# Kernel optimization log

Hardware: AMD Instinct MI355X
Metric: run time of the kernel (lower is better)

Reference implementation:

```python
import jax, jax.numpy as jnp
import numpy as np

N_NODES = 10000
N_EDGES = 50000
H = 64  # hidden channels


def _glorot(key, shape):
    fan_in = shape[0]
    return jax.random.normal(key, shape, dtype=jnp.float32) / jnp.sqrt(jnp.float32(fan_in))


def setup_inputs() -> dict:
    key = jax.random.key(0)
    ks = jax.random.split(key, 16)
    x = jax.random.normal(ks[0], (N_NODES, 20), dtype=jnp.float32)
    edge_index = jax.random.randint(ks[1], (2, N_EDGES), 0, N_NODES, dtype=jnp.int64)
    edge_attr = jax.random.uniform(ks[2], (N_EDGES, 5), dtype=jnp.float32)
    vpa = jax.random.normal(ks[3], (1,), dtype=jnp.float32)
    mz = jax.random.normal(ks[4], (1,), dtype=jnp.float32)
    adduct = jax.random.normal(ks[5], (3,), dtype=jnp.float32)
    params = {
        'lin0_w': _glorot(ks[6], (20, H)), 'lin0_b': jnp.zeros((H,), jnp.float32),
        'nn1_w': _glorot(ks[7], (5, H)), 'nn1_b': jnp.zeros((H,), jnp.float32),
        'nn2_w': _glorot(ks[8], (H, H * H)), 'nn2_b': jnp.zeros((H * H,), jnp.float32),
        'root_w': _glorot(ks[9], (H, H)), 'conv_b': jnp.zeros((H,), jnp.float32),
        'bneck_w': _glorot(ks[10], (H + 2 + 3, 384)), 'bneck_b': jnp.zeros((384,), jnp.float32),
        'lin1_w': _glorot(ks[11], (384, 384)), 'lin1_b': jnp.zeros((384,), jnp.float32),
        'lin2_w': _glorot(ks[12], (384, 1)), 'lin2_b': jnp.zeros((1,), jnp.float32),
    }
    return dict(x=x, edge_index=edge_index, edge_attr=edge_attr, vpa=vpa, mz=mz,
                adduct=adduct, **params)


def reference(x, edge_index, edge_attr, vpa, mz, adduct,
              lin0_w, lin0_b, nn1_w, nn1_b, nn2_w, nn2_b, root_w, conv_b,
              bneck_w, bneck_b, lin1_w, lin1_b, lin2_w, lin2_b):
    n = x.shape[0]
    src, dst = edge_index[0], edge_index[1]

    h = jax.nn.relu(x @ lin0_w + lin0_b)  # [N,64]

    # Edge-conditioned weights (edge_attr is loop-invariant -> compute once).
    e_hidden = jax.nn.relu(edge_attr @ nn1_w + nn1_b)          # [E,64]
    w_edge = (e_hidden @ nn2_w + nn2_b).reshape(-1, H, H)      # [E,64,64]

    # mean-aggregation denominator (in-degree, clamped to >=1)
    deg = jax.ops.segment_sum(jnp.ones_like(dst, dtype=h.dtype), dst,
                              num_segments=n)
    denom = jnp.maximum(deg, 1.0)[:, None]                     # [N,1]

    for _ in range(3):  # graph_conv_N
        msg = jnp.einsum('ei,eio->eo', h[src], w_edge)         # [E,64]
        agg = jax.ops.segment_sum(msg, dst, num_segments=n) / denom
        h = jax.nn.relu(h @ root_w + agg + conv_b)

    out_g = jnp.sum(h, axis=0)                                  # [64]
    out = jnp.concatenate([out_g, vpa, mz, adduct], axis=-1)    # [69]
    out = jax.nn.relu(out @ bneck_w + bneck_b)                  # [384]
    for _ in range(6):  # MLP_N
        out = jax.nn.relu(out @ lin1_w + lin1_b)
    return out @ lin2_w + lin2_b                                # [1]
```

## Files before the change

### kernel.cpp

```cpp
#include <hip/hip_runtime.h>
#include <stdint.h>

#define NN 10000
#define NE 50000
#define KTOT 4224
#define SPLITK 11
#define KCH 384
#define NSTEP 12
#define KPAD 200

typedef __attribute__((ext_vector_type(8))) _Float16 f16x8;
typedef __attribute__((ext_vector_type(4))) float f32x4;

__global__ void k_lin0(const float* __restrict__ x, const float* __restrict__ w,
                       const float* __restrict__ b, float* __restrict__ h) {
  int idx = blockIdx.x * blockDim.x + threadIdx.x;
  if (idx >= NN * 64) return;
  int n = idx >> 6, o = idx & 63;
  float acc = b[o];
  const float* xr = x + n * 20;
#pragma unroll
  for (int j = 0; j < 20; ++j) acc += xr[j] * w[j * 64 + o];
  h[idx] = acc > 0.f ? acc : 0.f;
}

__global__ void k_eh(const float* __restrict__ ea, const float* __restrict__ w,
                     const float* __restrict__ b, float* __restrict__ u) {
  int idx = blockIdx.x * blockDim.x + threadIdx.x;
  if (idx >= NE * 64) return;
  int e = idx >> 6, o = idx & 63;
  float acc = b[o];
  const float* er = ea + e * 5;
#pragma unroll
  for (int j = 0; j < 5; ++j) acc += er[j] * w[j * 64 + o];
  u[idx] = acc > 0.f ? acc : 0.f;
}

__global__ void k_deg(const int* __restrict__ ei, int* __restrict__ deg) {
  int e = blockIdx.x * blockDim.x + threadIdx.x;
  if (e < NE) atomicAdd(&deg[ei[NE + e]], 1);
}

__global__ void k_scan(const int* __restrict__ deg, int* __restrict__ offs,
                       float* __restrict__ inv_denom) {
  __shared__ int s[256];
  int t = threadIdx.x;
  int base = t * 40;
  int sum = 0;
  for (int j = 0; j < 40; ++j) {
    int n = base + j;
    sum += (n < NN) ? deg[n] : 0;
  }
  s[t] = sum;
  __syncthreads();
  for (int off = 1; off < 256; off <<= 1) {
    int v = (t >= off) ? s[t - off] : 0;
    __syncthreads();
    s[t] += v;
    __syncthreads();
  }
  int run = s[t] - sum;
  for (int j = 0; j < 40; ++j) {
    int n = base + j;
    if (n < NN) {
      offs[n] = run;
      int d = deg[n];
      run += d;
      inv_denom[n] = 1.0f / (float)(d > 0 ? d : 1);
    }
  }
  if (t == 255) offs[NN] = s[255];
}

__global__ void k_csr(const int* __restrict__ ei, const int* __restrict__ offs,
                      int* __restrict__ cursor, int* __restrict__ csr_src,
                      int* __restrict__ csr_eid) {
  int e = blockIdx.x * blockDim.x + threadIdx.x;
  if (e >= NE) return;
  int d = ei[NE + e];
  int pos = offs[d] + atomicAdd(&cursor[d], 1);
  csr_src[pos] = ei[e];
  csr_eid[pos] = e;
}

__global__ void k_wf(const float* __restrict__ w2, const float* __restrict__ b2,
                     const float* __restrict__ rootw, _Float16* __restrict__ wh,
                     _Float16* __restrict__ wl) {
  int idx = blockIdx.x * blockDim.x + threadIdx.x;
  if (idx >= 64 * KTOT) return;
  int o = idx / KTOT, c = idx - o * KTOT;
  float v;
  if (c < 4096) {
    v = w2[(c >> 6) * 4096 + (c & 63) * 64 + o];
  } else if (c < 4160) {
    v = b2[(c - 4096) * 64 + o];
  } else {
    v = rootw[(c - 4160) * 64 + o];
  }
  _Float16 hi = (_Float16)v;
  wh[idx] = hi;
  wl[idx] = (_Float16)(v - (float)hi);
}

__global__ void __launch_bounds__(256) k_scatter(
    const float* __restrict__ h, const float* __restrict__ u,
    const int* __restrict__ offs, const int* __restrict__ csr_src,
    const int* __restrict__ csr_eid, const float* __restrict__ inv_denom,
    _Float16* __restrict__ sv16, int chunk_start, int chunk_nodes) {
  __shared__ float hrow_s[4][2][64];
  int t = threadIdx.x;
  int wid = t >> 6, lane = t & 63;
  int n_local = blockIdx.x * 4 + wid;
  if (n_local >= chunk_nodes) return;
  int n = chunk_start + n_local;
  int beg = offs[n], end = offs[n + 1];
  int nE = end - beg;
  float invd = inv_denom[n];
  float acc[64];
#pragma unroll
  for (int i = 0; i < 64; ++i) acc[i] = 0.f;
  float hsacc = 0.f;
  float uk_c = 0.f, hv_c = 0.f;
  int eid_n = 0, src_n = 0;
  if (nE > 0) {
    int e0 = csr_eid[beg], s0 = csr_src[beg];
    uk_c = u[(size_t)e0 * 64 + lane];
    hv_c = h[(size_t)s0 * 64 + lane];
    hrow_s[wid][0][lane] = hv_c;
    if (nE > 1) { eid_n = csr_eid[beg + 1]; src_n = csr_src[beg + 1]; }
  }
  for (int c = 0; c < nE; ++c) {
    float uk_nn = 0.f, hv_nn = 0.f;
    if (c + 1 < nE) {
      uk_nn = u[(size_t)eid_n * 64 + lane];
      hv_nn = h[(size_t)src_n * 64 + lane];
    }
    if (c + 2 < nE) { eid_n = csr_eid[beg + c + 2]; src_n = csr_src[beg + c + 2]; }
    hsacc += hv_c;
    float uk = uk_c;
    const float* rowp = &hrow_s[wid][c & 1][0];
#pragma unroll
    for (int j = 0; j < 16; ++j) {
      float4 h4 = *(const float4*)&rowp[j * 4];
      acc[j * 4 + 0] += uk * h4.x;
      acc[j * 4 + 1] += uk * h4.y;
      acc[j * 4 + 2] += uk * h4.z;
      acc[j * 4 + 3] += uk * h4.w;
    }
    if (c + 1 < nE) hrow_s[wid][(c + 1) & 1][lane] = hv_nn;
    uk_c = uk_nn; hv_c = hv_nn;
  }
  size_t rowo = (size_t)n_local * KTOT + (size_t)lane * 64;
#pragma unroll
  for (int j = 0; j < 8; ++j) {
    f16x8 v;
#pragma unroll
    for (int q = 0; q < 8; ++q) v[q] = (_Float16)(acc[j * 8 + q] * invd);
    *(f16x8*)(sv16 + rowo + j * 8) = v;
  }
  size_t base = (size_t)n_local * KTOT;
  sv16[base + 4096 + lane] = (_Float16)(hsacc * invd);
  sv16[base + 4160 + lane] = (_Float16)(h[(size_t)n * 64 + lane]);
}

__global__ void __launch_bounds__(256) k_mfma(
    const _Float16* __restrict__ sv16, const _Float16* __restrict__ wh,
    const _Float16* __restrict__ wl, float* __restrict__ part,
    int chunk_start, int chunk_nodes) {
  __shared__ _Float16 Bh_s[64 * KPAD];
  __shared__ _Float16 Bl_s[64 * KPAD];
  int t = threadIdx.x;
  int wid = t >> 6, lane = t & 63;
  int node0 = blockIdx.x * 128;
  int kc = blockIdx.y;
  int r16 = lane & 15, kg = lane >> 4;
  int row0 = node0 + wid * 16 + r16;
  int row1 = row0 + 64;
  int rg0 = row0 < chunk_nodes ? row0 : (chunk_nodes - 1);
  int rg1 = row1 < chunk_nodes ? row1 : (chunk_nodes - 1);
  const _Float16* pa0 = sv16 + (size_t)rg0 * KTOT + kg * 8;
  const _Float16* pa1 = sv16 + (size_t)rg1 * KTOT + kg * 8;
  f32x4 p0 = {0.f, 0.f, 0.f, 0.f}, p1 = p0, p2 = p0, p3 = p0;
  f32x4 q0 = p0, q1 = p0, q2 = p0, q3 = p0;
  const int kb0 = kc * KCH;
  f16x8 a0 = *(const f16x8*)(pa0 + kb0);
  f16x8 a1 = *(const f16x8*)(pa1 + kb0);
  const int lb = r16 * KPAD + kg * 8;
#pragma unroll 1
  for (int ks = 0; ks < NSTEP; ++ks) {
    if ((ks == 0) || (ks == 6)) {
      __syncthreads();
      int gb = kb0 + (ks >> 1) * 32 * 0 + (ks / 6) * 192;
#pragma unroll
      for (int j = 0; j < 6; ++j) {
        int c = j * 256 + t;
        int o = c / 24, kk = (c - o * 24) * 8;
        *(f16x8*)&Bh_s[o * KPAD + kk] = *(const f16x8*)&wh[(size_t)o * KTOT + gb + kk];
        *(f16x8*)&Bl_s[o * KPAD + kk] = *(const f16x8*)&wl[(size_t)o * KTOT + gb + kk];
      }
      __syncthreads();
    }
    int kb = kb0 + ks * 32;
    int kbn = kb + ((ks + 1 < NSTEP) ? 32 : 0);
    int lk = lb + (ks % 6) * 32;
    f16x8 bh0 = *(const f16x8*)&Bh_s[lk];
    f16x8 bh1 = *(const f16x8*)&Bh_s[lk + 16 * KPAD];
    f16x8 bh2 = *(const f16x8*)&Bh_s[lk + 32 * KPAD];
    f16x8 bh3 = *(const f16x8*)&Bh_s[lk + 48 * KPAD];
    f16x8 bl0 = *(const f16x8*)&Bl_s[lk];
    f16x8 bl1 = *(const f16x8*)&Bl_s[lk + 16 * KPAD];
    f16x8 bl2 = *(const f16x8*)&Bl_s[lk + 32 * KPAD];
    f16x8 bl3 = *(const f16x8*)&Bl_s[lk + 48 * KPAD];
    f16x8 n0 = *(const f16x8*)(pa0 + kbn);
    f16x8 n1 = *(const f16x8*)(pa1 + kbn);
    p0 = __builtin_amdgcn_mfma_f32_16x16x32_f16(a0, bh0, p0, 0, 0, 0);
    p1 = __builtin_amdgcn_mfma_f32_16x16x32_f16(a0, bh1, p1, 0, 0, 0);
    p2 = __builtin_amdgcn_mfma_f32_16x16x32_f16(a0, bh2, p2, 0, 0, 0);
    p3 = __builtin_amdgcn_mfma_f32_16x16x32_f16(a0, bh3, p3, 0, 0, 0);
    p0 = __builtin_amdgcn_mfma_f32_16x16x32_f16(a0, bl0, p0, 0, 0, 0);
    p1 = __builtin_amdgcn_mfma_f32_16x16x32_f16(a0, bl1, p1, 0, 0, 0);
    p2 = __builtin_amdgcn_mfma_f32_16x16x32_f16(a0, bl2, p2, 0, 0, 0);
    p3 = __builtin_amdgcn_mfma_f32_16x16x32_f16(a0, bl3, p3, 0, 0, 0);
    q0 = __builtin_amdgcn_mfma_f32_16x16x32_f16(a1, bh0, q0, 0, 0, 0);
    q1 = __builtin_amdgcn_mfma_f32_16x16x32_f16(a1, bh1, q1, 0, 0, 0);
    q2 = __builtin_amdgcn_mfma_f32_16x16x32_f16(a1, bh2, q2, 0, 0, 0);
    q3 = __builtin_amdgcn_mfma_f32_16x16x32_f16(a1, bh3, q3, 0, 0, 0);
    q0 = __builtin_amdgcn_mfma_f32_16x16x32_f16(a1, bl0, q0, 0, 0, 0);
    q1 = __builtin_amdgcn_mfma_f32_16x16x32_f16(a1, bl1, q1, 0, 0, 0);
    q2 = __builtin_amdgcn_mfma_f32_16x16x32_f16(a1, bl2, q2, 0, 0, 0);
    q3 = __builtin_amdgcn_mfma_f32_16x16x32_f16(a1, bl3, q3, 0, 0, 0);
    a0 = n0; a1 = n1;
  }
  float* pp0 = part + (size_t)kc * NN * 64 +
               (size_t)(chunk_start + node0 + wid * 16) * 64;
  float* pp1 = pp0 + (size_t)64 * 64;
  int rbase = kg * 4;
#pragma unroll
  for (int j = 0; j < 4; ++j) {
    int row = rbase + j;
    if (node0 + wid * 16 + row < chunk_nodes) {
      pp0[row * 64 + 0  + r16] = p0[j];
      pp0[row * 64 + 16 + r16] = p1[j];
      pp0[row * 64 + 32 + r16] = p2[j];
      pp0[row * 64 + 48 + r16] = p3[j];
    }
    if (node0 + 64 + wid * 16 + row < chunk_nodes) {
      pp1[row * 64 + 0  + r16] = q0[j];
      pp1[row * 64 + 16 + r16] = q1[j];
      pp1[row * 64 + 32 + r16] = q2[j];
      pp1[row * 64 + 48 + r16] = q3[j];
    }
  }
}

__global__ void k_epi(const float* __restrict__ part, const float* __restrict__ cb,
                      float* __restrict__ hout) {
  int idx4 = blockIdx.x * blockDim.x + threadIdx.x;
  if (idx4 >= NN * 16) return;
  int o4 = (idx4 & 15) * 4;
  float4 a = make_float4(cb[o4], cb[o4 + 1], cb[o4 + 2], cb[o4 + 3]);
#pragma unroll
  for (int kc = 0; kc < SPLITK; ++kc) {
    float4 pv = *(const float4*)&part[(size_t)kc * NN * 64 + (size_t)idx4 * 4];
    a.x += pv.x; a.y += pv.y; a.z += pv.z; a.w += pv.w;
  }
  float4 r = make_float4(a.x > 0.f ? a.x : 0.f, a.y > 0.f ? a.y : 0.f,
                         a.z > 0.f ? a.z : 0.f, a.w > 0.f ? a.w : 0.f);
  *(float4*)&hout[(size_t)idx4 * 4] = r;
}

__global__ void k_sum_p(const float* __restrict__ h, float* __restrict__ part) {
  __shared__ float s[256];
  int t = threadIdx.x, b = blockIdx.x;
  int o = t & 63, g = t >> 6;
  float acc = 0.f;
  for (int k = 0;; ++k) {
    int n = b + 160 * (g + 4 * k);
    if (n >= NN) break;
    acc += h[(size_t)n * 64 + o];
  }
  s[t] = acc;
  __syncthreads();
  if (t < 64) part[(size_t)b * 64 + t] = s[t] + s[64 + t] + s[128 + t] + s[192 + t];
}

__global__ void __launch_bounds__(384) k_bneck(
    const float* __restrict__ part, const float* __restrict__ vpa,
    const float* __restrict__ mz, const float* __restrict__ adduct,
    const float* __restrict__ bw, const float* __restrict__ bb,
    float* __restrict__ aout) {
  __shared__ float in69[69];
  __shared__ float red[256];
  int t = threadIdx.x;
  if (t < 256) {
    int o = t & 63, g = t >> 6;
    float acc = 0.f;
    for (int k = 0; k < 40; ++k) acc += part[(size_t)(g * 40 + k) * 64 + o];
    red[t] = acc;
  }
  __syncthreads();
  if (t < 64) in69[t] = red[t] + red[64 + t] + red[128 + t] + red[192 + t];
  if (t == 64) in69[64] = vpa[0];
  if (t == 65) in69[65] = mz[0];
  if (t >= 66 && t < 69) in69[t] = adduct[t - 66];
  __syncthreads();
  float acc = bb[t];
#pragma unroll 4
  for (int i = 0; i < 69; ++i) acc += in69[i] * bw[i * 384 + t];
  aout[t] = acc > 0.f ? acc : 0.f;
}

__global__ void __launch_bounds__(256) k_layer(
    const float* __restrict__ ain, const float* __restrict__ w,
    const float* __restrict__ bias, float* __restrict__ aout) {
  __shared__ float a_s[384];
  __shared__ float red[256];
  int t = threadIdx.x;
  for (int i = t; i < 384; i += 256) a_s[i] = ain[i];
  __syncthreads();
  int o = blockIdx.x * 16 + (t & 15);
  int ig = t >> 4;
  float acc = 0.f;
#pragma unroll
  for (int k = 0; k < 24; ++k) {
    int i = ig + (k << 4);
    acc += a_s[i] * w[i * 384 + o];
  }
  red[t] = acc;
  __syncthreads();
  if (t < 128) red[t] += red[t + 128];
  __syncthreads();
  if (t < 64) red[t] += red[t + 64];
  __syncthreads();
  if (t < 32) red[t] += red[t + 32];
  __syncthreads();
  if (t < 16) {
    float v = red[t] + red[t + 16] + bias[o];
    aout[o] = v > 0.f ? v : 0.f;
  }
}

__global__ void __launch_bounds__(384) k_out(
    const float* __restrict__ act, const float* __restrict__ l2w,
    const float* __restrict__ l2b, float* __restrict__ out) {
  __shared__ float red[384];
  int t = threadIdx.x;
  red[t] = act[t] * l2w[t];
  __syncthreads();
  if (t < 128) red[t] += red[t + 128] + red[t + 256];
  __syncthreads();
  if (t < 64) {
    float s2 = red[t] + red[t + 64];
#pragma unroll
    for (int off = 32; off; off >>= 1) s2 += __shfl_down(s2, off);
    if (t == 0) out[0] = s2 + l2b[0];
  }
}

extern "C" void kernel_launch(void* const* d_in, const int* in_sizes, int n_in,
                              void* d_out, int out_size, void* d_ws, size_t ws_size,
                              hipStream_t stream) {
  const float* x      = (const float*)d_in[0];
  const int* ei       = (const int*)d_in[1];
  const float* ea     = (const float*)d_in[2];
  const float* vpa    = (const float*)d_in[3];
  const float* mz     = (const float*)d_in[4];
  const float* adduct = (const float*)d_in[5];
  const float* lin0_w = (const float*)d_in[6];
  const float* lin0_b = (const float*)d_in[7];
  const float* nn1_w  = (const float*)d_in[8];
  const float* nn1_b  = (const float*)d_in[9];
  const float* nn2_w  = (const float*)d_in[10];
  const float* nn2_b  = (const float*)d_in[11];
  const float* root_w = (const float*)d_in[12];
  const float* conv_b = (const float*)d_in[13];
  const float* bw     = (const float*)d_in[14];
  const float* bb     = (const float*)d_in[15];
  const float* l1w    = (const float*)d_in[16];
  const float* l1b    = (const float*)d_in[17];
  const float* l2w    = (const float*)d_in[18];
  const float* l2b    = (const float*)d_in[19];

  char* p = (char*)d_ws;
  auto alloc = [&](size_t bytes) {
    char* r = p;
    p += (bytes + 255) & ~(size_t)255;
    return r;
  };
  float* h0      = (float*)alloc((size_t)NN * 64 * 4);
  float* h1      = (float*)alloc((size_t)NN * 64 * 4);
  float* u       = (float*)alloc((size_t)NE * 64 * 4);
  _Float16* wh   = (_Float16*)alloc((size_t)64 * KTOT * 2);
  _Float16* wl   = (_Float16*)alloc((size_t)64 * KTOT * 2);
  int* deg       = (int*)alloc(NN * 4);
  int* offs      = (int*)alloc((NN + 1) * 4);
  int* cursor    = (int*)alloc(NN * 4);
  float* invd    = (float*)alloc(NN * 4);
  int* csr_src   = (int*)alloc(NE * 4);
  int* csr_eid   = (int*)alloc(NE * 4);
  float* part    = (float*)alloc(160 * 64 * 4);
  float* kpart   = (float*)alloc((size_t)SPLITK * NN * 64 * 4);
  float* actA    = (float*)alloc(384 * 4);
  float* actB    = (float*)alloc(384 * 4);
  size_t used = (size_t)(p - (char*)d_ws);
  size_t avail = ws_size > used ? ws_size - used : 0;
  long long CH = (long long)(avail / ((size_t)KTOT * 2));
  if (CH > NN) CH = NN;
  if (CH < 1) CH = 1;
  _Float16* sv16 = (_Float16*)p;

  hipMemsetAsync(deg, 0, NN * 4, stream);
  hipMemsetAsync(cursor, 0, NN * 4, stream);

  k_lin0<<<(NN * 64 + 255) / 256, 256, 0, stream>>>(x, lin0_w, lin0_b, h0);
  k_eh<<<(NE * 64 + 255) / 256, 256, 0, stream>>>(ea, nn1_w, nn1_b, u);
  k_deg<<<(NE + 255) / 256, 256, 0, stream>>>(ei, deg);
  k_scan<<<1, 256, 0, stream>>>(deg, offs, invd);
  k_csr<<<(NE + 255) / 256, 256, 0, stream>>>(ei, offs, cursor, csr_src, csr_eid);
  k_wf<<<(64 * KTOT + 255) / 256, 256, 0, stream>>>(nn2_w, nn2_b, root_w, wh, wl);

  float* hc = h0;
  float* hn = h1;
  for (int it = 0; it < 3; ++it) {
    for (int cs = 0; cs < NN; cs += (int)CH) {
      int cn = (NN - cs < (int)CH) ? (NN - cs) : (int)CH;
      k_scatter<<<(cn + 3) / 4, 256, 0, stream>>>(hc, u, offs, csr_src, csr_eid,
                                                  invd, sv16, cs, cn);
      dim3 g2((cn + 127) / 128, SPLITK);
      k_mfma<<<g2, 256, 0, stream>>>(sv16, wh, wl, kpart, cs, cn);
    }
    k_epi<<<(NN * 16 + 255) / 256, 256, 0, stream>>>(kpart, conv_b, hn);
    float* tmp = hc; hc = hn; hn = tmp;
  }
  k_sum_p<<<160, 256, 0, stream>>>(hc, part);
  k_bneck<<<1, 384, 0, stream>>>(part, vpa, mz, adduct, bw, bb, actA);
  float* ain = actA;
  float* aout = actB;
  for (int L = 0; L < 6; ++L) {
    k_layer<<<24, 256, 0, stream>>>(ain, l1w, l1b, aout);
    float* tmp = ain; ain = aout; aout = tmp;
  }
  k_out<<<1, 384, 0, stream>>>(ain, l2w, l2b, (float*)d_out);
}
```

Baseline: 296.9 us.

## Fuse split-K epilogue into MFMA kernel, merge front kernels, unroll scatter by two

The split-K reduction plus bias and ReLU epilogue moves into k_mfma. The last-arriving K-split block per row tile, found with an atomic counter, sums the partials and writes h, which removes one launch per iteration. The lin0 and edge-hidden kernels are merged into one launch, and the two memsets are combined into one by placing deg, cursor and done next to each other. The scatter kernel now uses 128-thread blocks and handles two edges per loop step for more memory-level parallelism. The trade-offs are a threadfence and atomic per block, a serialized tail reduction done by only 11-way last blocks, and done[] is 80 entries, which assumes at most 80 row tiles.

```diff
diff --git a/kernel.cpp b/kernel.cpp
--- a/kernel.cpp
+++ b/kernel.cpp
@@ -12,28 +12,28 @@
 typedef __attribute__((ext_vector_type(8))) _Float16 f16x8;
 typedef __attribute__((ext_vector_type(4))) float f32x4;
 
-__global__ void k_lin0(const float* __restrict__ x, const float* __restrict__ w,
-                       const float* __restrict__ b, float* __restrict__ h) {
+__global__ void k_front(const float* __restrict__ x, const float* __restrict__ l0w,
+                        const float* __restrict__ l0b, const float* __restrict__ ea,
+                        const float* __restrict__ n1w, const float* __restrict__ n1b,
+                        float* __restrict__ h, float* __restrict__ u) {
   int idx = blockIdx.x * blockDim.x + threadIdx.x;
-  if (idx >= NN * 64) return;
-  int n = idx >> 6, o = idx & 63;
-  float acc = b[o];
-  const float* xr = x + n * 20;
-#pragma unroll
-  for (int j = 0; j < 20; ++j) acc += xr[j] * w[j * 64 + o];
-  h[idx] = acc > 0.f ? acc : 0.f;
-}
-
-__global__ void k_eh(const float* __restrict__ ea, const float* __restrict__ w,
-                     const float* __restrict__ b, float* __restrict__ u) {
-  int idx = blockIdx.x * blockDim.x + threadIdx.x;
-  if (idx >= NE * 64) return;
-  int e = idx >> 6, o = idx & 63;
-  float acc = b[o];
-  const float* er = ea + e * 5;
-#pragma unroll
-  for (int j = 0; j < 5; ++j) acc += er[j] * w[j * 64 + o];
-  u[idx] = acc > 0.f ? acc : 0.f;
+  if (idx < NN * 64) {
+    int n = idx >> 6, o = idx & 63;
+    float acc = l0b[o];
+    const float* xr = x + n * 20;
+#pragma unroll
+    for (int j = 0; j < 20; ++j) acc += xr[j] * l0w[j * 64 + o];
+    h[idx] = acc > 0.f ? acc : 0.f;
+  } else {
+    int idx2 = idx - NN * 64;
+    if (idx2 >= NE * 64) return;
+    int e = idx2 >> 6, o = idx2 & 63;
+    float acc = n1b[o];
+    const float* er = ea + e * 5;
+#pragma unroll
+    for (int j = 0; j < 5; ++j) acc += er[j] * n1w[j * 64 + o];
+    u[idx2] = acc > 0.f ? acc : 0.f;
+  }
 }
 
 __global__ void k_deg(const int* __restrict__ ei, int* __restrict__ deg) {
@@ -102,15 +102,15 @@
   wl[idx] = (_Float16)(v - (float)hi);
 }
 
-__global__ void __launch_bounds__(256) k_scatter(
+__global__ void __launch_bounds__(128) k_scatter(
     const float* __restrict__ h, const float* __restrict__ u,
     const int* __restrict__ offs, const int* __restrict__ csr_src,
     const int* __restrict__ csr_eid, const float* __restrict__ inv_denom,
     _Float16* __restrict__ sv16, int chunk_start, int chunk_nodes) {
-  __shared__ float hrow_s[4][2][64];
+  __shared__ float hrow[2][2][64];
   int t = threadIdx.x;
   int wid = t >> 6, lane = t & 63;
-  int n_local = blockIdx.x * 4 + wid;
+  int n_local = blockIdx.x * 2 + wid;
   if (n_local >= chunk_nodes) return;
   int n = chunk_start + n_local;
   int beg = offs[n], end = offs[n + 1];
@@ -120,35 +120,40 @@
 #pragma unroll
   for (int i = 0; i < 64; ++i) acc[i] = 0.f;
   float hsacc = 0.f;
-  float uk_c = 0.f, hv_c = 0.f;
-  int eid_n = 0, src_n = 0;
+  float u0 = 0.f, h0 = 0.f, u1 = 0.f, h1 = 0.f;
   if (nE > 0) {
-    int e0 = csr_eid[beg], s0 = csr_src[beg];
-    uk_c = u[(size_t)e0 * 64 + lane];
-    hv_c = h[(size_t)s0 * 64 + lane];
-    hrow_s[wid][0][lane] = hv_c;
-    if (nE > 1) { eid_n = csr_eid[beg + 1]; src_n = csr_src[beg + 1]; }
-  }
-  for (int c = 0; c < nE; ++c) {
-    float uk_nn = 0.f, hv_nn = 0.f;
-    if (c + 1 < nE) {
-      uk_nn = u[(size_t)eid_n * 64 + lane];
-      hv_nn = h[(size_t)src_n * 64 + lane];
-    }
-    if (c + 2 < nE) { eid_n = csr_eid[beg + c + 2]; src_n = csr_src[beg + c + 2]; }
-    hsacc += hv_c;
-    float uk = uk_c;
-    const float* rowp = &hrow_s[wid][c & 1][0];
+    int e = csr_eid[beg], s = csr_src[beg];
+    u0 = u[(size_t)e * 64 + lane]; h0 = h[(size_t)s * 64 + lane];
+  }
+  if (nE > 1) {
+    int e = csr_eid[beg + 1], s = csr_src[beg + 1];
+    u1 = u[(size_t)e * 64 + lane]; h1 = h[(size_t)s * 64 + lane];
+  }
+  for (int c = 0; c < nE; c += 2) {
+    hrow[wid][0][lane] = h0;
+    hrow[wid][1][lane] = h1;
+    bool two = (c + 1 < nE);
+    hsacc += h0 + (two ? h1 : 0.f);
+    float uk0 = u0, uk1 = two ? u1 : 0.f;
+    float nu0 = 0.f, nh0 = 0.f, nu1 = 0.f, nh1 = 0.f;
+    if (c + 2 < nE) {
+      int e = csr_eid[beg + c + 2], s = csr_src[beg + c + 2];
+      nu0 = u[(size_t)e * 64 + lane]; nh0 = h[(size_t)s * 64 + lane];
+    }
+    if (c + 3 < nE) {
+      int e = csr_eid[beg + c + 3], s = csr_src[beg + c + 3];
+      nu1 = u[(size_t)e * 64 + lane]; nh1 = h[(size_t)s * 64 + lane];
+    }
 #pragma unroll
     for (int j = 0; j < 16; ++j) {
-      float4 h4 = *(const float4*)&rowp[j * 4];
-      acc[j * 4 + 0] += uk * h4.x;
-      acc[j * 4 + 1] += uk * h4.y;
-      acc[j * 4 + 2] += uk * h4.z;
-      acc[j * 4 + 3] += uk * h4.w;
-    }
-    if (c + 1 < nE) hrow_s[wid][(c + 1) & 1][lane] = hv_nn;
-    uk_c = uk_nn; hv_c = hv_nn;
+      float4 a4 = *(const float4*)&hrow[wid][0][j * 4];
+      float4 b4 = *(const float4*)&hrow[wid][1][j * 4];
+      acc[j * 4 + 0] += uk0 * a4.x + uk1 * b4.x;
+      acc[j * 4 + 1] += uk0 * a4.y + uk1 * b4.y;
+      acc[j * 4 + 2] += uk0 * a4.z + uk1 * b4.z;
+      acc[j * 4 + 3] += uk0 * a4.w + uk1 * b4.w;
+    }
+    u0 = nu0; h0 = nh0; u1 = nu1; h1 = nh1;
   }
   size_t rowo = (size_t)n_local * KTOT + (size_t)lane * 64;
 #pragma unroll
@@ -165,10 +170,12 @@
 
 __global__ void __launch_bounds__(256) k_mfma(
     const _Float16* __restrict__ sv16, const _Float16* __restrict__ wh,
-    const _Float16* __restrict__ wl, float* __restrict__ part,
-    int chunk_start, int chunk_nodes) {
+    const _Float16* __restrict__ wl, float* __restrict__ kpart,
+    float* __restrict__ hout, const float* __restrict__ cb,
+    int* __restrict__ done, int chunk_start, int chunk_nodes) {
   __shared__ _Float16 Bh_s[64 * KPAD];
   __shared__ _Float16 Bl_s[64 * KPAD];
+  __shared__ int sflag;
   int t = threadIdx.x;
   int wid = t >> 6, lane = t & 63;
   int node0 = blockIdx.x * 128;
@@ -190,7 +197,7 @@
   for (int ks = 0; ks < NSTEP; ++ks) {
     if ((ks == 0) || (ks == 6)) {
       __syncthreads();
-      int gb = kb0 + (ks >> 1) * 32 * 0 + (ks / 6) * 192;
+      int gb = kb0 + (ks / 6) * 192;
 #pragma unroll
       for (int j = 0; j < 6; ++j) {
         int c = j * 256 + t;
@@ -231,7 +238,7 @@
     q3 = __builtin_amdgcn_mfma_f32_16x16x32_f16(a1, bl3, q3, 0, 0, 0);
     a0 = n0; a1 = n1;
   }
-  float* pp0 = part + (size_t)kc * NN * 64 +
+  float* pp0 = kpart + (size_t)kc * NN * 64 +
                (size_t)(chunk_start + node0 + wid * 16) * 64;
   float* pp1 = pp0 + (size_t)64 * 64;
   int rbase = kg * 4;
@@ -251,22 +258,31 @@
       pp1[row * 64 + 48 + r16] = q3[j];
     }
   }
-}
-
-__global__ void k_epi(const float* __restrict__ part, const float* __restrict__ cb,
-                      float* __restrict__ hout) {
-  int idx4 = blockIdx.x * blockDim.x + threadIdx.x;
-  if (idx4 >= NN * 16) return;
-  int o4 = (idx4 & 15) * 4;
-  float4 a = make_float4(cb[o4], cb[o4 + 1], cb[o4 + 2], cb[o4 + 3]);
-#pragma unroll
-  for (int kc = 0; kc < SPLITK; ++kc) {
-    float4 pv = *(const float4*)&part[(size_t)kc * NN * 64 + (size_t)idx4 * 4];
-    a.x += pv.x; a.y += pv.y; a.z += pv.z; a.w += pv.w;
-  }
-  float4 r = make_float4(a.x > 0.f ? a.x : 0.f, a.y > 0.f ? a.y : 0.f,
-                         a.z > 0.f ? a.z : 0.f, a.w > 0.f ? a.w : 0.f);
-  *(float4*)&hout[(size_t)idx4 * 4] = r;
+  __threadfence();
+  if (t == 0) {
+    int prev = __hip_atomic_fetch_add(&done[blockIdx.x], 1, __ATOMIC_ACQ_REL,
+                                      __HIP_MEMORY_SCOPE_AGENT);
+    sflag = (prev == SPLITK - 1) ? 1 : 0;
+  }
+  __syncthreads();
+  if (sflag) {
+    if (t == 0) done[blockIdx.x] = 0;
+    for (int j4 = t; j4 < 2048; j4 += 256) {
+      int node = node0 + (j4 >> 4);
+      if (node >= chunk_nodes) break;
+      int o4 = (j4 & 15) * 4;
+      float4 a = make_float4(cb[o4], cb[o4 + 1], cb[o4 + 2], cb[o4 + 3]);
+      size_t off = (size_t)(chunk_start + node) * 64 + o4;
+#pragma unroll
+      for (int kc2 = 0; kc2 < SPLITK; ++kc2) {
+        float4 pv = *(const float4*)&kpart[(size_t)kc2 * NN * 64 + off];
+        a.x += pv.x; a.y += pv.y; a.z += pv.z; a.w += pv.w;
+      }
+      float4 r = make_float4(a.x > 0.f ? a.x : 0.f, a.y > 0.f ? a.y : 0.f,
+                             a.z > 0.f ? a.z : 0.f, a.w > 0.f ? a.w : 0.f);
+      *(float4*)&hout[off] = r;
+    }
+  }
 }
 
 __global__ void k_sum_p(const float* __restrict__ h, float* __restrict__ part) {
@@ -393,8 +409,10 @@
   _Float16* wh   = (_Float16*)alloc((size_t)64 * KTOT * 2);
   _Float16* wl   = (_Float16*)alloc((size_t)64 * KTOT * 2);
   int* deg       = (int*)alloc(NN * 4);
+  int* cursor    = (int*)alloc(NN * 4);
+  int* done      = (int*)alloc(80 * 4);
+  size_t zero_bytes = (size_t)((char*)(done + 80) - (char*)deg);
   int* offs      = (int*)alloc((NN + 1) * 4);
-  int* cursor    = (int*)alloc(NN * 4);
   float* invd    = (float*)alloc(NN * 4);
   int* csr_src   = (int*)alloc(NE * 4);
   int* csr_eid   = (int*)alloc(NE * 4);
@@ -409,11 +427,10 @@
   if (CH < 1) CH = 1;
   _Float16* sv16 = (_Float16*)p;
 
-  hipMemsetAsync(deg, 0, NN * 4, stream);
-  hipMemsetAsync(cursor, 0, NN * 4, stream);
-
-  k_lin0<<<(NN * 64 + 255) / 256, 256, 0, stream>>>(x, lin0_w, lin0_b, h0);
-  k_eh<<<(NE * 64 + 255) / 256, 256, 0, stream>>>(ea, nn1_w, nn1_b, u);
+  hipMemsetAsync(deg, 0, zero_bytes, stream);
+
+  k_front<<<(NN * 64 + NE * 64 + 255) / 256, 256, 0, stream>>>(
+      x, lin0_w, lin0_b, ea, nn1_w, nn1_b, h0, u);
   k_deg<<<(NE + 255) / 256, 256, 0, stream>>>(ei, deg);
   k_scan<<<1, 256, 0, stream>>>(deg, offs, invd);
   k_csr<<<(NE + 255) / 256, 256, 0, stream>>>(ei, offs, cursor, csr_src, csr_eid);
@@ -424,12 +441,11 @@
   for (int it = 0; it < 3; ++it) {
     for (int cs = 0; cs < NN; cs += (int)CH) {
       int cn = (NN - cs < (int)CH) ? (NN - cs) : (int)CH;
-      k_scatter<<<(cn + 3) / 4, 256, 0, stream>>>(hc, u, offs, csr_src, csr_eid,
+      k_scatter<<<(cn + 1) / 2, 128, 0, stream>>>(hc, u, offs, csr_src, csr_eid,
                                                   invd, sv16, cs, cn);
       dim3 g2((cn + 127) / 128, SPLITK);
-      k_mfma<<<g2, 256, 0, stream>>>(sv16, wh, wl, kpart, cs, cn);
-    }
-    k_epi<<<(NN * 16 + 255) / 256, 256, 0, stream>>>(kpart, conv_b, hn);
+      k_mfma<<<g2, 256, 0, stream>>>(sv16, wh, wl, kpart, hn, conv_b, done, cs, cn);
+    }
     float* tmp = hc; hc = hn; hn = tmp;
   }
   k_sum_p<<<160, 256, 0, stream>>>(hc, part);
```

New measurement: 716.4 us. 2.41x slower.
